# Performance work log

Measured on AMD Instinct MI355X. Metric: run time of the kernel, lower is better.

The kernel has to match this reference:

```python
import jax, jax.numpy as jnp
import numpy as np

MAX_SPAN_WIDTH = 30
NUM_WORDS = 2048
NUM_CAND = 8192
HIDDEN = 768
FEAT = 20
FFNN = 1000
SPAN_DIM = HIDDEN * 3 + FEAT  # 2324
TOP_SPAN_NUM = int(NUM_WORDS * 0.4)  # 819


def setup_inputs() -> dict:
    key = jax.random.key(0)
    ks = jax.random.split(key, 16)
    mention_doc = jax.random.normal(ks[0], (NUM_WORDS, HIDDEN), jnp.float32)
    starts = jax.random.randint(ks[1], (NUM_CAND,), 0, NUM_WORDS - MAX_SPAN_WIDTH, jnp.int32)
    widths = jax.random.randint(ks[2], (NUM_CAND,), 1, MAX_SPAN_WIDTH + 1, jnp.int32)
    ends = jnp.minimum(starts + widths - 1, NUM_WORDS - 1).astype(jnp.int32)
    s = 0.02
    lin = lambda k, i, o: jax.random.normal(k, (i, o), jnp.float32) * s
    return dict(
        mention_doc=mention_doc,
        span_width_emb=jax.random.normal(ks[3], (MAX_SPAN_WIDTH, FEAT), jnp.float32) * s,
        head_w=jax.random.normal(ks[4], (HIDDEN,), jnp.float32) * s,
        head_b=jnp.zeros((), jnp.float32),
        m_w1=lin(ks[5], SPAN_DIM, FFNN), m_b1=jnp.zeros((FFNN,), jnp.float32),
        m_w2=lin(ks[6], FFNN, FFNN), m_b2=jnp.zeros((FFNN,), jnp.float32),
        m_w3=jax.random.normal(ks[7], (FFNN,), jnp.float32) * s, m_b3=jnp.zeros((), jnp.float32),
        width_prior_emb=jax.random.normal(ks[8], (MAX_SPAN_WIDTH, FEAT), jnp.float32) * s,
        w_w1=lin(ks[9], FEAT, FFNN), w_b1=jnp.zeros((FFNN,), jnp.float32),
        w_w2=lin(ks[10], FFNN, FFNN), w_b2=jnp.zeros((FFNN,), jnp.float32),
        w_w3=jax.random.normal(ks[11], (FFNN,), jnp.float32) * s, w_b3=jnp.zeros((), jnp.float32),
        candidate_starts=starts,
        candidate_ends=ends,
        top_span_num=TOP_SPAN_NUM,
    )


def get_span_emb(mention_doc, starts, ends, span_width_emb, head_w, head_b):
    # mention_doc: [N, H]; starts/ends: [C]
    num_words = mention_doc.shape[0]
    start_emb = mention_doc[starts]              # [C, H]
    end_emb = mention_doc[ends]                  # [C, H]
    width_ids = ends - starts                    # span width - 1, in [0, MAX_SPAN_WIDTH)
    width_emb = span_width_emb[width_ids]        # [C, F]
    offs = jnp.arange(MAX_SPAN_WIDTH, dtype=starts.dtype)
    idxes = jnp.minimum(starts[:, None] + offs[None, :], num_words - 1)  # [C, W]
    emb_spans = mention_doc[idxes]               # [C, W, H]  (dominant intermediate)
    head_scores = mention_doc @ head_w + head_b  # [N]
    hs = head_scores[idxes]                      # [C, W]
    mask = offs[None, :] <= width_ids[:, None]
    hs = jnp.where(mask, hs, -jnp.inf)
    attn = jax.nn.softmax(hs, axis=1)            # masked softmax over span positions
    attended = jnp.einsum('cw,cwh->ch', attn, emb_spans)
    return jnp.concatenate([start_emb, end_emb, width_emb, attended], axis=-1)  # [C, 3H+F]


def ffnn3(x, w1, b1, w2, b2, w3, b3):
    h = jax.nn.relu(x @ w1 + b1)
    h = jax.nn.relu(h @ w2 + b2)
    return h @ w3 + b3  # [..., ] scalar score per row (Squeezer)


def extract_top_spans(span_scores, starts, ends, top_span_num, num_words):
    # Greedy crossing-interval NMS, faithful to the original sequential algorithm.
    C = span_scores.shape[0]
    order = jnp.argsort(-span_scores)
    offs = jnp.arange(MAX_SPAN_WIDTH, dtype=jnp.int32)

    def body(i, state):
        max_end, min_start, sel, count = state
        idx = order[i]
        s = starts[idx]
        e = ends[idx]
        dup = max_end[s] == e
        j_raw = s + offs
        j = jnp.minimum(j_raw, num_words - 1)
        in_span = j_raw <= e
        # crossing: an already-selected span starting at j>s ends beyond e,
        # or one ending at j<e starts before s.
        c1 = in_span & (j_raw > s) & (max_end[j] > e)
        c2 = in_span & (j_raw < e) & (min_start[j] < s)
        crossed = jnp.any(c1 | c2)
        accept = (~dup) & (~crossed) & (count < top_span_num)
        sel = jnp.where(accept, sel.at[count].set(idx.astype(jnp.int32)), sel)
        max_end = jnp.where(accept, max_end.at[s].max(e), max_end)
        min_start = jnp.where(accept, min_start.at[e].min(s), min_start)
        count = count + accept.astype(jnp.int32)
        return (max_end, min_start, sel, count)

    max_end0 = jnp.full((num_words,), -1, jnp.int32)          # 'not set' sentinel
    min_start0 = jnp.full((num_words,), num_words, jnp.int32)  # 'not set' sentinel
    sel0 = jnp.zeros((top_span_num,), jnp.int32)
    _, _, sel, count = jax.lax.fori_loop(0, C, body, (max_end0, min_start0, sel0, jnp.int32(0)))

    # sort selected spans by (start, end); pad unfilled slots with the first sorted span
    valid = jnp.arange(top_span_num) < count
    keys = jnp.where(valid, starts[sel] * num_words + ends[sel], jnp.iinfo(jnp.int32).max)
    sorted_sel = sel[jnp.argsort(keys)]
    return jnp.where(valid, sorted_sel, sorted_sel[0])


def reference(mention_doc, span_width_emb, head_w, head_b,
              m_w1, m_b1, m_w2, m_b2, m_w3, m_b3,
              width_prior_emb, w_w1, w_b1, w_w2, w_b2, w_w3, w_b3,
              candidate_starts, candidate_ends, top_span_num):
    num_words = mention_doc.shape[0]
    span_emb = get_span_emb(mention_doc, candidate_starts, candidate_ends,
                            span_width_emb, head_w, head_b)            # [C, 2324]
    mention_scores = ffnn3(span_emb, m_w1, m_b1, m_w2, m_b2, m_w3, m_b3)  # [C]
    width_scores = ffnn3(width_prior_emb, w_w1, w_b1, w_w2, w_b2, w_w3, w_b3)  # [30]
    cand_mention_scores = mention_scores + width_scores[candidate_ends - candidate_starts]
    top_idx = extract_top_spans(cand_mention_scores, candidate_starts, candidate_ends,
                                top_span_num, num_words)               # [top]
    top_starts = candidate_starts[top_idx]
    top_ends = candidate_ends[top_idx]
    top_span_emb = span_emb[top_idx]
    top_scores = cand_mention_scores[top_idx]
    return (cand_mention_scores, top_idx, top_starts, top_ends, top_span_emb, top_scores)
```

## Files before the change

### kernel.cpp

```cpp
#include <hip/hip_runtime.h>
#include <cstdio>
#include <cmath>

#define NUM_WORDS 2048
#define NUM_CAND 8192
#define HIDDEN 768
#define FEAT 20
#define FFNN_DIM 1000
#define SPAN_DIM 2324
#define TOP_NUM 819
#define MSW 30
#define KP2 1024
#define NP 1024
#define PNP 3072

#define OUT_TOPIDX   (NUM_CAND)
#define OUT_TSTART   (NUM_CAND + TOP_NUM)
#define OUT_TEND     (NUM_CAND + 2*TOP_NUM)
#define OUT_TEMB     (NUM_CAND + 3*TOP_NUM)
#define OUT_TSCORE   (NUM_CAND + 3*TOP_NUM + TOP_NUM*SPAN_DIM)

typedef short short8 __attribute__((ext_vector_type(8)));
typedef float f32x4 __attribute__((ext_vector_type(4)));

__device__ __forceinline__ unsigned short bf16_rne(float x) {
    unsigned int u = __float_as_uint(x);
    unsigned int r = u + 0x7FFFu + ((u >> 16) & 1u);
    return (unsigned short)(r >> 16);
}
__device__ __forceinline__ float bf16_to_f(unsigned short h) {
    return __uint_as_float(((unsigned int)h) << 16);
}
__device__ __forceinline__ void store_split3(unsigned short* p0, unsigned short* p1,
                                             unsigned short* p2, size_t off, float v) {
    unsigned short h0 = bf16_rne(v);
    float r1 = v - bf16_to_f(h0);
    unsigned short h1 = bf16_rne(r1);
    float r2 = r1 - bf16_to_f(h1);
    p0[off] = h0;
    p1[off] = h1;
    p2[off] = bf16_rne(r2);
}

__device__ __forceinline__ void gl_lds16(const unsigned short* g, unsigned short* l) {
    __builtin_amdgcn_global_load_lds(
        (const __attribute__((address_space(1))) unsigned short*)g,
        (__attribute__((address_space(3))) unsigned short*)l, 16, 0, 0);
}

__global__ void head_kernel(const float* __restrict__ doc, const float* __restrict__ hw,
                            const float* __restrict__ hb, float* __restrict__ out) {
    int wave = threadIdx.x >> 6, lane = threadIdx.x & 63;
    int row = blockIdx.x * 4 + wave;
    if (row >= NUM_WORDS) return;
    float acc = 0.f;
    for (int h = lane; h < HIDDEN; h += 64) acc += doc[row * HIDDEN + h] * hw[h];
    for (int off = 32; off > 0; off >>= 1) acc += __shfl_down(acc, off);
    if (lane == 0) out[row] = acc + hb[0];
}

__global__ void width_kernel(const float* __restrict__ x, const float* __restrict__ w1,
                             const float* __restrict__ b1, const float* __restrict__ w2,
                             const float* __restrict__ b2, const float* __restrict__ w3,
                             const float* __restrict__ b3, float* __restrict__ out) {
    __shared__ float xs[FEAT];
    __shared__ float h1s[FFNN_DIM];
    __shared__ float red[256];
    int r = blockIdx.x, t = threadIdx.x;
    if (t < FEAT) xs[t] = x[r * FEAT + t];
    __syncthreads();
    for (int j = t; j < FFNN_DIM; j += 256) {
        float acc = b1[j];
        for (int k = 0; k < FEAT; ++k) acc += xs[k] * w1[k * FFNN_DIM + j];
        h1s[j] = fmaxf(acc, 0.f);
    }
    __syncthreads();
    float partial = 0.f;
    for (int j = t; j < FFNN_DIM; j += 256) {
        float acc = b2[j];
        for (int k = 0; k < FFNN_DIM; ++k) acc += h1s[k] * w2[k * FFNN_DIM + j];
        partial += fmaxf(acc, 0.f) * w3[j];
    }
    red[t] = partial;
    __syncthreads();
    for (int s = 128; s > 0; s >>= 1) { if (t < s) red[t] += red[t + s]; __syncthreads(); }
    if (t == 0) out[r] = red[0] + b3[0];
}

__global__ void attn_kernel(const float* __restrict__ head_s, const int* __restrict__ starts,
                            const int* __restrict__ ends, float* __restrict__ attn_g) {
    int wave = threadIdx.x >> 6, w = threadIdx.x & 63;
    int c = blockIdx.x * 4 + wave;
    if (c >= NUM_CAND) return;
    int s = starts[c], e = ends[c];
    int wid = e - s;
    float hsv = -INFINITY;
    if (w < MSW && w <= wid) hsv = head_s[s + w];
    float m = hsv;
    for (int off = 32; off > 0; off >>= 1) m = fmaxf(m, __shfl_down(m, off));
    m = __shfl(m, 0);
    float ex = (w < MSW && w <= wid) ? expf(hsv - m) : 0.f;
    float ssum = ex;
    for (int off = 32; off > 0; off >>= 1) ssum += __shfl_down(ssum, off);
    ssum = __shfl(ssum, 0);
    if (w < 32) attn_g[c * 32 + w] = (w < MSW) ? (ex / ssum) : 0.f;
}

__global__ void doc_convert(const float* __restrict__ doc, unsigned short* __restrict__ d0,
                            unsigned short* __restrict__ d1, unsigned short* __restrict__ d2) {
    int i = blockIdx.x * 256 + threadIdx.x;
    if (i < NUM_WORDS * HIDDEN) store_split3(d0, d1, d2, i, doc[i]);
}

__global__ void convert_wt(const float* __restrict__ w, int K, int N, int Kp,
                           unsigned short* __restrict__ q0, unsigned short* __restrict__ q1,
                           unsigned short* __restrict__ q2) {
    int n = blockIdx.y;
    int k = blockIdx.x * blockDim.x + threadIdx.x;
    if (k >= Kp) return;
    float v = (k < K && n < N) ? w[(size_t)k * N + n] : 0.f;
    store_split3(q0, q1, q2, (size_t)n * Kp + k, v);
}

__global__ void tw_kernel(const float* __restrict__ swe, const float* __restrict__ w1,
                          float* __restrict__ tw) {
    int wid = blockIdx.x, t = threadIdx.x;
    for (int n = t; n < NP; n += 256) {
        float acc = 0.f;
        if (n < FFNN_DIM) {
            for (int f = 0; f < FEAT; ++f)
                acc += swe[wid * FEAT + f] * w1[(size_t)(1536 + f) * FFNN_DIM + n];
        }
        tw[wid * NP + n] = acc;
    }
}

__device__ __forceinline__ void stage_tile(const unsigned short* __restrict__ src,
                                           unsigned short* lds, int base_row, int Kp, int k0,
                                           int t) {
#pragma unroll
    for (int qi = 0; qi < 2; ++qi) {
        int u = qi * 256 + t;
        int l = u & 63;
        int row = ((u >> 6) << 4) + (l >> 2);
        int cblk = (l & 3) ^ (row & 3);
        const unsigned short* g = src + (size_t)(base_row + row) * Kp + k0 + cblk * 8;
        gl_lds16(g, lds + u * 8);
    }
}

__global__ __launch_bounds__(256, 2) void gemm6p(
    const unsigned short* __restrict__ A0, const unsigned short* __restrict__ A1,
    const unsigned short* __restrict__ A2,
    const unsigned short* __restrict__ B0, const unsigned short* __restrict__ B1,
    const unsigned short* __restrict__ B2,
    float* __restrict__ C) {
    __shared__ unsigned short As0[128 * 32], As1[128 * 32], As2[128 * 32];
    __shared__ unsigned short Bs0[128 * 32], Bs1[128 * 32], Bs2[128 * 32];
    int t = threadIdx.x;
    int bid = blockIdx.x;
    int bm = (bid & 15) << 7;
    int bn = (bid >> 4) << 7;
    int lane = t & 63, wv = t >> 6;
    int wm = (wv >> 1) * 64, wn = (wv & 1) * 64;
    int lr = lane & 15, qq = lane >> 4;
    int sw = (qq ^ (lr & 3)) * 8;

    f32x4 acc[4][4] = {};

    for (int k0 = 0; k0 < HIDDEN; k0 += 32) {
        stage_tile(A0, As0, bm, HIDDEN, k0, t);
        stage_tile(A1, As1, bm, HIDDEN, k0, t);
        stage_tile(A2, As2, bm, HIDDEN, k0, t);
        stage_tile(B0, Bs0, bn, HIDDEN, k0, t);
        stage_tile(B1, Bs1, bn, HIDDEN, k0, t);
        stage_tile(B2, Bs2, bn, HIDDEN, k0, t);
        __syncthreads();
        short8 a0[4], a1[4], a2[4];
#pragma unroll
        for (int i = 0; i < 4; ++i) {
            int ra = (wm + i * 16 + lr) * 32 + sw;
            a0[i] = *(const short8*)&As0[ra];
            a1[i] = *(const short8*)&As1[ra];
            a2[i] = *(const short8*)&As2[ra];
        }
#pragma unroll
        for (int j = 0; j < 4; ++j) {
            int rb = (wn + j * 16 + lr) * 32 + sw;
            short8 b0 = *(const short8*)&Bs0[rb];
            short8 b1 = *(const short8*)&Bs1[rb];
            short8 b2 = *(const short8*)&Bs2[rb];
#pragma unroll
            for (int i = 0; i < 4; ++i) {
                acc[i][j] = __builtin_amdgcn_mfma_f32_16x16x32_bf16(a2[i], b0, acc[i][j], 0, 0, 0);
                acc[i][j] = __builtin_amdgcn_mfma_f32_16x16x32_bf16(a0[i], b2, acc[i][j], 0, 0, 0);
                acc[i][j] = __builtin_amdgcn_mfma_f32_16x16x32_bf16(a1[i], b1, acc[i][j], 0, 0, 0);
                acc[i][j] = __builtin_amdgcn_mfma_f32_16x16x32_bf16(a1[i], b0, acc[i][j], 0, 0, 0);
                acc[i][j] = __builtin_amdgcn_mfma_f32_16x16x32_bf16(a0[i], b1, acc[i][j], 0, 0, 0);
                acc[i][j] = __builtin_amdgcn_mfma_f32_16x16x32_bf16(a0[i], b0, acc[i][j], 0, 0, 0);
            }
        }
        __syncthreads();
    }
#pragma unroll
    for (int i = 0; i < 4; ++i)
#pragma unroll
        for (int j = 0; j < 4; ++j)
#pragma unroll
            for (int r = 0; r < 4; ++r) {
                int m = bm + wm + i * 16 + qq * 4 + r;
                int n = bn + wn + j * 16 + lr;
                C[(size_t)m * PNP + n] = acc[i][j][r];
            }
}

__global__ void combine_kernel(const float* __restrict__ P, const float* __restrict__ tw,
                               const float* __restrict__ attn_g, const float* __restrict__ b1,
                               const int* __restrict__ starts, const int* __restrict__ ends,
                               unsigned short* __restrict__ h0, unsigned short* __restrict__ h1,
                               unsigned short* __restrict__ h2) {
    int c = blockIdx.x, t = threadIdx.x;
    int s = starts[c], e = ends[c];
    int wid = e - s;
    __shared__ float at[MSW];
    if (t < MSW) at[t] = attn_g[c * 32 + t];
    __syncthreads();
    const float* Ps = P + (size_t)s * PNP;
    const float* Pe = P + (size_t)e * PNP + 1024;
    const float* Pa = P + (size_t)s * PNP + 2048;
    const float* Tw = tw + (size_t)wid * NP;
    for (int n = t; n < NP; n += 256) {
        if (n < FFNN_DIM) {
            float acc = Ps[n] + Pe[n] + Tw[n] + b1[n];
            for (int w = 0; w <= wid; ++w) acc += at[w] * Pa[(size_t)w * PNP + n];
            store_split3(h0, h1, h2, (size_t)c * NP + n, fmaxf(acc, 0.f));
        } else {
            h0[(size_t)c * NP + n] = 0;
            h1[(size_t)c * NP + n] = 0;
            h2[(size_t)c * NP + n] = 0;
        }
    }
}

__global__ __launch_bounds__(256, 2) void gemm6(
    const unsigned short* __restrict__ A0, const unsigned short* __restrict__ A1,
    const unsigned short* __restrict__ A2,
    const unsigned short* __restrict__ B0, const unsigned short* __restrict__ B1,
    const unsigned short* __restrict__ B2,
    const float* __restrict__ bias, int nreal, int Kp,
    const float* __restrict__ w3, float* __restrict__ partials) {
    __shared__ unsigned short As0[128 * 32], As1[128 * 32], As2[128 * 32];
    __shared__ unsigned short Bs0[128 * 32], Bs1[128 * 32], Bs2[128 * 32];
    int t = threadIdx.x;
    int bid = blockIdx.x;
    int sm = bid >> 6, idx = bid & 63;
    int bm = ((sm << 3) + (idx & 7)) << 7;
    int bn = (idx >> 3) << 7;
    int lane = t & 63, wv = t >> 6;
    int wm = (wv >> 1) * 64, wn = (wv & 1) * 64;
    int lr = lane & 15, qq = lane >> 4;
    int sw = (qq ^ (lr & 3)) * 8;

    f32x4 acc[4][4] = {};

    for (int k0 = 0; k0 < Kp; k0 += 32) {
        stage_tile(A0, As0, bm, Kp, k0, t);
        stage_tile(A1, As1, bm, Kp, k0, t);
        stage_tile(A2, As2, bm, Kp, k0, t);
        stage_tile(B0, Bs0, bn, Kp, k0, t);
        stage_tile(B1, Bs1, bn, Kp, k0, t);
        stage_tile(B2, Bs2, bn, Kp, k0, t);
        __syncthreads();
        short8 a0[4], a1[4], a2[4];
#pragma unroll
        for (int i = 0; i < 4; ++i) {
            int ra = (wm + i * 16 + lr) * 32 + sw;
            a0[i] = *(const short8*)&As0[ra];
            a1[i] = *(const short8*)&As1[ra];
            a2[i] = *(const short8*)&As2[ra];
        }
#pragma unroll
        for (int j = 0; j < 4; ++j) {
            int rb = (wn + j * 16 + lr) * 32 + sw;
            short8 b0 = *(const short8*)&Bs0[rb];
            short8 b1 = *(const short8*)&Bs1[rb];
            short8 b2 = *(const short8*)&Bs2[rb];
#pragma unroll
            for (int i = 0; i < 4; ++i) {
                acc[i][j] = __builtin_amdgcn_mfma_f32_16x16x32_bf16(a2[i], b0, acc[i][j], 0, 0, 0);
                acc[i][j] = __builtin_amdgcn_mfma_f32_16x16x32_bf16(a0[i], b2, acc[i][j], 0, 0, 0);
                acc[i][j] = __builtin_amdgcn_mfma_f32_16x16x32_bf16(a1[i], b1, acc[i][j], 0, 0, 0);
                acc[i][j] = __builtin_amdgcn_mfma_f32_16x16x32_bf16(a1[i], b0, acc[i][j], 0, 0, 0);
                acc[i][j] = __builtin_amdgcn_mfma_f32_16x16x32_bf16(a0[i], b1, acc[i][j], 0, 0, 0);
                acc[i][j] = __builtin_amdgcn_mfma_f32_16x16x32_bf16(a0[i], b0, acc[i][j], 0, 0, 0);
            }
        }
        __syncthreads();
    }

    int pid = ((bn >> 7) << 1) | (wn >> 6);
#pragma unroll
    for (int i = 0; i < 4; ++i)
#pragma unroll
        for (int r = 0; r < 4; ++r) {
            float p = 0.f;
#pragma unroll
            for (int j = 0; j < 4; ++j) {
                int n = bn + wn + j * 16 + lr;
                float v = acc[i][j][r] + (n < nreal ? bias[n] : 0.f);
                v = fmaxf(v, 0.f);
                p += v * (n < nreal ? w3[n] : 0.f);
            }
            p += __shfl_xor(p, 1);
            p += __shfl_xor(p, 2);
            p += __shfl_xor(p, 4);
            p += __shfl_xor(p, 8);
            if (lr == 0) {
                int m = bm + wm + i * 16 + qq * 4 + r;
                partials[(size_t)m * 16 + pid] = p;
            }
        }
}

__global__ void score_final(const float* __restrict__ partials, const float* __restrict__ b3,
                            const float* __restrict__ width_s, const int* __restrict__ starts,
                            const int* __restrict__ ends, float* __restrict__ out) {
    int c = blockIdx.x * 256 + threadIdx.x;
    if (c >= NUM_CAND) return;
    float s = b3[0] + width_s[ends[c] - starts[c]];
#pragma unroll
    for (int p = 0; p < 16; ++p) s += partials[(size_t)c * 16 + p];
    out[c] = s;
}

__global__ __launch_bounds__(256) void rank_kernel(const float* __restrict__ scores,
                                                   const int* __restrict__ starts,
                                                   const int* __restrict__ ends,
                                                   unsigned short* __restrict__ ord_g,
                                                   unsigned int* __restrict__ se_g) {
    __shared__ unsigned long long kk[NUM_CAND];
    int t = threadIdx.x;
    for (int i = t; i < NUM_CAND; i += 256) {
        unsigned int b = __float_as_uint(scores[i]);
        unsigned int u = b ^ ((b & 0x80000000u) ? 0xFFFFFFFFu : 0x80000000u);
        unsigned int hi = ~u;
        kk[i] = ((unsigned long long)hi << 32) | (unsigned int)i;
    }
    __syncthreads();
    int c = blockIdx.x * 32 + (t >> 3);
    int seg = (t & 7) * 1024;
    unsigned long long mykey = kk[c];
    int cnt = 0;
    for (int i = seg; i < seg + 1024; ++i) cnt += (kk[i] < mykey) ? 1 : 0;
    cnt += __shfl_xor(cnt, 1);
    cnt += __shfl_xor(cnt, 2);
    cnt += __shfl_xor(cnt, 4);
    if ((t & 7) == 0) {
        int idx = (int)(mykey & 0xFFFFFFFFull);
        int rank = cnt;
        ord_g[rank] = (unsigned short)idx;
        se_g[rank] = ((unsigned int)starts[idx] << 16) | (unsigned int)ends[idx];
    }
}

__global__ __launch_bounds__(512)
__attribute__((amdgpu_waves_per_eu(1, 2)))
void select_nms(const unsigned int* __restrict__ se_g,
                unsigned short* __restrict__ sel_g,
                int* __restrict__ count_g) {
    __shared__ unsigned int se_arr[NUM_CAND];
    __shared__ unsigned int st[2 * NUM_WORDS];
    __shared__ unsigned int lst[512];
    __shared__ int pos[9];
    __shared__ int count_sh;
    int t = threadIdx.x;
    int wv = t >> 6, lane = t & 63;

    for (int i = t; i < NUM_CAND; i += 512) se_arr[i] = se_g[i];
    for (int i = t; i < 2 * NUM_WORDS; i += 512)
        st[i] = (i & 1) ? (unsigned int)NUM_WORDS : 0u;
    if (t == 0) count_sh = 0;
    __syncthreads();

    const unsigned long long* stp = (const unsigned long long*)st;
    for (int r = 0; r < NUM_CAND / 512; ++r) {
        int ib = r * 512 + wv * 64;
        unsigned int sev = se_arr[ib + lane];
        int s = (int)(sev >> 16), e = (int)(sev & 0xFFFFu);
        const unsigned long long* bp = stp + s;
        unsigned long long v[MSW];
#pragma unroll
        for (int w = 0; w < MSW; ++w) v[w] = bp[w];
        int me = (int)(unsigned int)v[0] - 1;
        bool crossed = (s < e) && ((int)(unsigned int)(v[0] >> 32) < s);
#pragma unroll
        for (int w = 1; w < MSW; ++w) {
            int j = s + w;
            bool in = (j <= e);
            int mej = (int)(unsigned int)v[w] - 1;
            int msj = (int)(unsigned int)(v[w] >> 32);
            crossed = crossed || (in && ((mej > e) || ((j < e) && (msj < s))));
        }
        bool spec = !crossed && (me != e);
        if (t == 0) pos[0] = 0;
        __syncthreads();

        for (int p = 0; p < 8; ++p) {
            if (p > 0 && wv >= p) {
                int lo = pos[p - 1], hi = pos[p];
                for (int k = lo; k < hi; ++k) {
                    unsigned int sef = lst[k];
                    int sf = (int)(sef >> 16), ef = (int)(sef & 0xFFFFu);
                    if (s == sf) me = max(me, ef);
                    crossed = crossed || ((s < sf) && (sf <= e) && (ef > e))
                                      || ((sf < s) && (s <= ef) && (ef < e));
                }
                spec = !crossed && (me != e);
            }
            if (wv == p) {
                int cbefore = count_sh;
                int lbase = pos[p];
                if (cbefore < TOP_NUM) {
                    int count = cbefore;
                    unsigned long long window = ~0ull;
                    unsigned int pend = 0u;
                    int rk = 0, lcnt = 0;
                    while (true) {
                        unsigned long long b = __ballot(spec) & window;
                        if (b == 0ull) break;
                        int f = __ffsll((unsigned long long)b) - 1;
                        unsigned int sef = __builtin_amdgcn_readlane(sev, (unsigned int)f);
                        int sf = (int)(sef >> 16), ef = (int)(sef & 0xFFFFu);
                        bool mine = (lane == lcnt);
                        pend = mine ? sef : pend;
                        rk = mine ? (ib + f) : rk;
                        lcnt++;
                        count++;
                        if (count >= TOP_NUM) break;
                        window &= (f >= 63) ? 0ull : (~0ull << (f + 1));
                        if (lane > f) {
                            if (s == sf) me = max(me, ef);
                            crossed = crossed || ((s < sf) && (sf <= e) && (ef > e))
                                              || ((sf < s) && (s <= ef) && (ef < e));
                            spec = !crossed && (me != e);
                        }
                    }
                    if (lane < lcnt) {
                        int sf = (int)(pend >> 16), ef = (int)(pend & 0xFFFFu);
                        sel_g[cbefore + lane] = (unsigned short)rk;
                        lst[lbase + lane] = pend;
                        atomicMax(&st[2 * sf], (unsigned int)(ef + 1));
                        atomicMin(&st[2 * ef + 1], (unsigned int)sf);
                    }
                    if (lane == 0) {
                        count_sh = count;
                        pos[p + 1] = lbase + lcnt;
                    }
                } else {
                    if (lane == 0) pos[p + 1] = lbase;
                }
            }
            __syncthreads();
        }
        if (count_sh >= TOP_NUM) break;
    }
    if (t == 0) *count_g = count_sh;
}

__global__ __launch_bounds__(256) void select_post(const float* __restrict__ scores,
                                                   const int* __restrict__ starts,
                                                   const int* __restrict__ ends,
                                                   const unsigned short* __restrict__ ord_g,
                                                   const unsigned short* __restrict__ sel_g,
                                                   const int* __restrict__ count_g,
                                                   float* out, int* top_idx_ws) {
    __shared__ unsigned long long fkeys[1024];
    int t = threadIdx.x;
    int count = *count_g;
    for (int i = t; i < 1024; i += 256) {
        unsigned long long k = 0xFFFFFFFFFFFFFFFFull;
        if (i < count) {
            int idx = (int)ord_g[sel_g[i]];
            unsigned int key32 = (unsigned int)(starts[idx] * NUM_WORDS + ends[idx]);
            k = ((unsigned long long)key32 << 32) | (unsigned int)idx;
        }
        fkeys[i] = k;
    }
    __syncthreads();
    for (int size = 2; size <= 1024; size <<= 1) {
        for (int stride = size >> 1; stride > 0; stride >>= 1) {
            for (int i = t; i < 1024; i += 256) {
                int ixj = i ^ stride;
                if (ixj > i) {
                    bool up = ((i & size) == 0);
                    unsigned long long a = fkeys[i], b = fkeys[ixj];
                    if ((a > b) == up) { fkeys[i] = b; fkeys[ixj] = a; }
                }
            }
            __syncthreads();
        }
    }
    for (int i = t; i < TOP_NUM; i += 256) {
        int fi = (i < count) ? (int)(fkeys[i] & 0xFFFFFFFFull)
                             : (int)(fkeys[0] & 0xFFFFFFFFull);
        out[OUT_TOPIDX + i] = (float)fi;
        out[OUT_TSTART + i] = (float)starts[fi];
        out[OUT_TEND + i] = (float)ends[fi];
        out[OUT_TSCORE + i] = scores[fi];
        top_idx_ws[i] = fi;
    }
}

__global__ void gather_emb(const float* __restrict__ doc, const float* __restrict__ swe,
                           const float* __restrict__ attn_g, const int* __restrict__ starts,
                           const int* __restrict__ ends, const int* __restrict__ top_idx_ws,
                           float* __restrict__ out) {
    int r = blockIdx.x, t = threadIdx.x;
    int idx = top_idx_ws[r];
    int s = starts[idx], e = ends[idx];
    int wid = e - s;
    __shared__ float at[MSW];
    if (t < MSW) at[t] = attn_g[(size_t)idx * 32 + t];
    __syncthreads();
    float* dst = out + OUT_TEMB + (size_t)r * SPAN_DIM;
    for (int h = t; h < HIDDEN; h += 256) {
        dst[h] = doc[(size_t)s * HIDDEN + h];
        dst[HIDDEN + h] = doc[(size_t)e * HIDDEN + h];
        float acc = 0.f;
        for (int w = 0; w <= wid; ++w) acc += at[w] * doc[(size_t)(s + w) * HIDDEN + h];
        dst[2 * HIDDEN + FEAT + h] = acc;
    }
    if (t < FEAT) dst[2 * HIDDEN + t] = swe[wid * FEAT + t];
}

extern "C" void kernel_launch(void* const* d_in, const int* in_sizes, int n_in,
                              void* d_out, int out_size, void* d_ws, size_t ws_size,
                              hipStream_t stream) {
    const float* mention_doc = (const float*)d_in[0];
    const float* span_width_emb = (const float*)d_in[1];
    const float* head_w = (const float*)d_in[2];
    const float* head_b = (const float*)d_in[3];
    const float* m_w1 = (const float*)d_in[4];
    const float* m_b1 = (const float*)d_in[5];
    const float* m_w2 = (const float*)d_in[6];
    const float* m_b2 = (const float*)d_in[7];
    const float* m_w3 = (const float*)d_in[8];
    const float* m_b3 = (const float*)d_in[9];
    const float* width_prior_emb = (const float*)d_in[10];
    const float* w_w1 = (const float*)d_in[11];
    const float* w_b1 = (const float*)d_in[12];
    const float* w_w2 = (const float*)d_in[13];
    const float* w_b2 = (const float*)d_in[14];
    const float* w_w3 = (const float*)d_in[15];
    const float* w_b3 = (const float*)d_in[16];
    const int* cand_starts = (const int*)d_in[17];
    const int* cand_ends = (const int*)d_in[18];

    char* w = (char*)d_ws;
    const size_t szH = (size_t)NUM_CAND * NP * 2;
    const size_t szW2 = (size_t)NP * KP2 * 2;
    const size_t szWc = (size_t)PNP * HIDDEN * 2;
    const size_t szD = (size_t)NUM_WORDS * HIDDEN * 2;
    char* p = w;
    unsigned short* h0 = (unsigned short*)p; p += szH;
    unsigned short* h1 = (unsigned short*)p; p += szH;
    unsigned short* h2 = (unsigned short*)p; p += szH;
    unsigned short* w2t0 = (unsigned short*)p; p += szW2;
    unsigned short* w2t1 = (unsigned short*)p; p += szW2;
    unsigned short* w2t2 = (unsigned short*)p; p += szW2;
    unsigned short* Wc0 = (unsigned short*)p; p += szWc;
    unsigned short* Wc1 = (unsigned short*)p; p += szWc;
    unsigned short* Wc2 = (unsigned short*)p; p += szWc;
    unsigned short* d0 = (unsigned short*)p; p += szD;
    unsigned short* d1 = (unsigned short*)p; p += szD;
    unsigned short* d2 = (unsigned short*)p; p += szD;
    float* P = (float*)p; p += (size_t)NUM_WORDS * PNP * 4;
    float* tw = (float*)p; p += (size_t)MSW * NP * 4;
    float* attn_g = (float*)p; p += (size_t)NUM_CAND * 32 * 4;
    float* partials = (float*)p; p += (size_t)NUM_CAND * 16 * 4;
    unsigned short* ord_g = (unsigned short*)p; p += (size_t)NUM_CAND * 2;
    unsigned int* se_g = (unsigned int*)p; p += (size_t)NUM_CAND * 4;
    unsigned short* sel_g = (unsigned short*)p; p += 2048;
    int* count_g = (int*)p; p += 128;
    float* head_s = (float*)p; p += NUM_WORDS * 4;
    float* width_s = (float*)p; p += 128;
    int* top_idx_ws = (int*)p; p += 4096;

    size_t need = (size_t)(p - w);
    if (ws_size < need) {
        fprintf(stderr, "kernel_launch: ws too small (%zu < %zu)\n", ws_size, need);
    }

    float* out = (float*)d_out;

    head_kernel<<<NUM_WORDS / 4, 256, 0, stream>>>(mention_doc, head_w, head_b, head_s);
    width_kernel<<<MSW, 256, 0, stream>>>(width_prior_emb, w_w1, w_b1, w_w2, w_b2, w_w3, w_b3,
                                          width_s);
    attn_kernel<<<NUM_CAND / 4, 256, 0, stream>>>(head_s, cand_starts, cand_ends, attn_g);
    doc_convert<<<(NUM_WORDS * HIDDEN + 255) / 256, 256, 0, stream>>>(mention_doc, d0, d1, d2);
    convert_wt<<<dim3(3, 1024), 256, 0, stream>>>(m_w1, HIDDEN, FFNN_DIM, HIDDEN,
                                                  Wc0, Wc1, Wc2);
    convert_wt<<<dim3(3, 1024), 256, 0, stream>>>(m_w1 + (size_t)HIDDEN * FFNN_DIM, HIDDEN,
                                                  FFNN_DIM, HIDDEN,
                                                  Wc0 + (size_t)1024 * HIDDEN,
                                                  Wc1 + (size_t)1024 * HIDDEN,
                                                  Wc2 + (size_t)1024 * HIDDEN);
    convert_wt<<<dim3(3, 1024), 256, 0, stream>>>(m_w1 + (size_t)1556 * FFNN_DIM, HIDDEN,
                                                  FFNN_DIM, HIDDEN,
                                                  Wc0 + (size_t)2048 * HIDDEN,
                                                  Wc1 + (size_t)2048 * HIDDEN,
                                                  Wc2 + (size_t)2048 * HIDDEN);
    convert_wt<<<dim3(4, 1024), 256, 0, stream>>>(m_w2, FFNN_DIM, FFNN_DIM, KP2,
                                                  w2t0, w2t1, w2t2);
    tw_kernel<<<MSW, 256, 0, stream>>>(span_width_emb, m_w1, tw);
    gemm6p<<<16 * 24, 256, 0, stream>>>(d0, d1, d2, Wc0, Wc1, Wc2, P);
    combine_kernel<<<NUM_CAND, 256, 0, stream>>>(P, tw, attn_g, m_b1, cand_starts, cand_ends,
                                                 h0, h1, h2);
    gemm6<<<512, 256, 0, stream>>>(h0, h1, h2, w2t0, w2t1, w2t2, m_b2, FFNN_DIM, KP2,
                                   m_w3, partials);
    score_final<<<NUM_CAND / 256, 256, 0, stream>>>(partials, m_b3, width_s, cand_starts,
                                                    cand_ends, out);
    rank_kernel<<<NUM_CAND / 32, 256, 0, stream>>>(out, cand_starts, cand_ends, ord_g, se_g);
    select_nms<<<1, 512, 0, stream>>>(se_g, sel_g, count_g);
    select_post<<<1, 256, 0, stream>>>(out, cand_starts, cand_ends, ord_g, sel_g, count_g,
                                       out, top_idx_ws);
    gather_emb<<<TOP_NUM, 256, 0, stream>>>(mention_doc, span_width_emb, attn_g, cand_starts,
                                            cand_ends, top_idx_ws, out);
}
```

Measured before the change: 900.6 us.

## Replace barrier-staged NMS rounds with flag-chained wave pipeline in select_nms

```diff
diff --git a/kernel.cpp b/kernel.cpp
--- a/kernel.cpp
+++ b/kernel.cpp
@@ -363,6 +363,9 @@
     }
 }
 
+#define NCHUNK (NUM_CAND / 64)
+#define FLAG_SENT 0xFFFFFFFFu
+
 __global__ __launch_bounds__(512)
 __attribute__((amdgpu_waves_per_eu(1, 2)))
 void select_nms(const unsigned int* __restrict__ se_g,
@@ -370,21 +373,32 @@
                 int* __restrict__ count_g) {
     __shared__ unsigned int se_arr[NUM_CAND];
     __shared__ unsigned int st[2 * NUM_WORDS];
-    __shared__ unsigned int lst[512];
-    __shared__ int pos[9];
-    __shared__ int count_sh;
+    __shared__ unsigned int lst[1024];
+    __shared__ unsigned int flagv[NCHUNK];
     int t = threadIdx.x;
     int wv = t >> 6, lane = t & 63;
 
     for (int i = t; i < NUM_CAND; i += 512) se_arr[i] = se_g[i];
     for (int i = t; i < 2 * NUM_WORDS; i += 512)
         st[i] = (i & 1) ? (unsigned int)NUM_WORDS : 0u;
-    if (t == 0) count_sh = 0;
+    if (t < NCHUNK) flagv[t] = FLAG_SENT;
     __syncthreads();
 
     const unsigned long long* stp = (const unsigned long long*)st;
-    for (int r = 0; r < NUM_CAND / 512; ++r) {
-        int ib = r * 512 + wv * 64;
+    unsigned int lo = 0;
+    for (int c = wv; c < NCHUNK; c += 8) {
+        int ib = c * 64;
+        if (c > 0) {
+            unsigned int pk = __hip_atomic_load(&flagv[c - 1], __ATOMIC_ACQUIRE,
+                                                __HIP_MEMORY_SCOPE_WORKGROUP);
+            if (pk != FLAG_SENT && pk >= TOP_NUM) {
+                if (lane == 0)
+                    __hip_atomic_store(&flagv[c], pk, __ATOMIC_RELEASE,
+                                       __HIP_MEMORY_SCOPE_WORKGROUP);
+                lo = pk;
+                continue;
+            }
+        }
         unsigned int sev = se_arr[ib + lane];
         int s = (int)(sev >> 16), e = (int)(sev & 0xFFFFu);
         const unsigned long long* bp = stp + s;
@@ -401,70 +415,73 @@
             int msj = (int)(unsigned int)(v[w] >> 32);
             crossed = crossed || (in && ((mej > e) || ((j < e) && (msj < s))));
         }
+        unsigned int prev = lo;
+        bool drained = false;
+        for (int d = (c >= 8) ? (c - 7) : 0; d < c; ++d) {
+            unsigned int hd;
+            while ((hd = __hip_atomic_load(&flagv[d], __ATOMIC_ACQUIRE,
+                                           __HIP_MEMORY_SCOPE_WORKGROUP)) == FLAG_SENT)
+                __builtin_amdgcn_s_sleep(1);
+            if (hd >= TOP_NUM) {
+                if (lane == 0)
+                    __hip_atomic_store(&flagv[c], hd, __ATOMIC_RELEASE,
+                                       __HIP_MEMORY_SCOPE_WORKGROUP);
+                lo = hd;
+                drained = true;
+                break;
+            }
+            for (unsigned int k = prev; k < hd; ++k) {
+                unsigned int sef = lst[k];
+                int sf = (int)(sef >> 16), ef = (int)(sef & 0xFFFFu);
+                if (s == sf) me = max(me, ef);
+                crossed = crossed || ((s < sf) && (sf <= e) && (ef > e))
+                                  || ((sf < s) && (s <= ef) && (ef < e));
+            }
+            prev = hd;
+        }
+        if (drained) continue;
         bool spec = !crossed && (me != e);
-        if (t == 0) pos[0] = 0;
-        __syncthreads();
-
-        for (int p = 0; p < 8; ++p) {
-            if (p > 0 && wv >= p) {
-                int lo = pos[p - 1], hi = pos[p];
-                for (int k = lo; k < hi; ++k) {
-                    unsigned int sef = lst[k];
-                    int sf = (int)(sef >> 16), ef = (int)(sef & 0xFFFFu);
-                    if (s == sf) me = max(me, ef);
-                    crossed = crossed || ((s < sf) && (sf <= e) && (ef > e))
-                                      || ((sf < s) && (s <= ef) && (ef < e));
-                }
+        unsigned int cbefore = prev;
+        int count = (int)cbefore;
+        __builtin_amdgcn_s_setprio(1);
+        unsigned long long window = ~0ull;
+        unsigned int pend = 0u;
+        int rk = 0, lcnt = 0;
+        while (true) {
+            unsigned long long b = __ballot(spec) & window;
+            if (b == 0ull) break;
+            int f = __ffsll((unsigned long long)b) - 1;
+            unsigned int sef = __builtin_amdgcn_readlane(sev, (unsigned int)f);
+            int sf = (int)(sef >> 16), ef = (int)(sef & 0xFFFFu);
+            bool mine = (lane == lcnt);
+            pend = mine ? sef : pend;
+            rk = mine ? (ib + f) : rk;
+            lcnt++;
+            count++;
+            if (count >= TOP_NUM) break;
+            window &= (f >= 63) ? 0ull : (~0ull << (f + 1));
+            if (lane > f) {
+                if (s == sf) me = max(me, ef);
+                crossed = crossed || ((s < sf) && (sf <= e) && (ef > e))
+                                  || ((sf < s) && (s <= ef) && (ef < e));
                 spec = !crossed && (me != e);
             }
-            if (wv == p) {
-                int cbefore = count_sh;
-                int lbase = pos[p];
-                if (cbefore < TOP_NUM) {
-                    int count = cbefore;
-                    unsigned long long window = ~0ull;
-                    unsigned int pend = 0u;
-                    int rk = 0, lcnt = 0;
-                    while (true) {
-                        unsigned long long b = __ballot(spec) & window;
-                        if (b == 0ull) break;
-                        int f = __ffsll((unsigned long long)b) - 1;
-                        unsigned int sef = __builtin_amdgcn_readlane(sev, (unsigned int)f);
-                        int sf = (int)(sef >> 16), ef = (int)(sef & 0xFFFFu);
-                        bool mine = (lane == lcnt);
-                        pend = mine ? sef : pend;
-                        rk = mine ? (ib + f) : rk;
-                        lcnt++;
-                        count++;
-                        if (count >= TOP_NUM) break;
-                        window &= (f >= 63) ? 0ull : (~0ull << (f + 1));
-                        if (lane > f) {
-                            if (s == sf) me = max(me, ef);
-                            crossed = crossed || ((s < sf) && (sf <= e) && (ef > e))
-                                              || ((sf < s) && (s <= ef) && (ef < e));
-                            spec = !crossed && (me != e);
-                        }
-                    }
-                    if (lane < lcnt) {
-                        int sf = (int)(pend >> 16), ef = (int)(pend & 0xFFFFu);
-                        sel_g[cbefore + lane] = (unsigned short)rk;
-                        lst[lbase + lane] = pend;
-                        atomicMax(&st[2 * sf], (unsigned int)(ef + 1));
-                        atomicMin(&st[2 * ef + 1], (unsigned int)sf);
-                    }
-                    if (lane == 0) {
-                        count_sh = count;
-                        pos[p + 1] = lbase + lcnt;
-                    }
-                } else {
-                    if (lane == 0) pos[p + 1] = lbase;
-                }
-            }
-            __syncthreads();
-        }
-        if (count_sh >= TOP_NUM) break;
-    }
-    if (t == 0) *count_g = count_sh;
+        }
+        __builtin_amdgcn_s_setprio(0);
+        if (lane < lcnt) {
+            int sf = (int)(pend >> 16), ef = (int)(pend & 0xFFFFu);
+            sel_g[cbefore + lane] = (unsigned short)rk;
+            lst[cbefore + lane] = pend;
+            atomicMax(&st[2 * sf], (unsigned int)(ef + 1));
+            atomicMin(&st[2 * ef + 1], (unsigned int)sf);
+        }
+        if (lane == 0)
+            __hip_atomic_store(&flagv[c], (unsigned int)count, __ATOMIC_RELEASE,
+                               __HIP_MEMORY_SCOPE_WORKGROUP);
+        lo = (unsigned int)count;
+    }
+    __syncthreads();
+    if (t == 0) *count_g = (int)flagv[NCHUNK - 1];
 }
 
 __global__ __launch_bounds__(256) void select_post(const float* __restrict__ scores,
```

Result: slower. 990.0 us (+9.9%).
